# Performance work log

Hardware: AMD Instinct MI355X
Metric: run time of the kernel (lower is better)

The kernel has to match this reference:

```python
import jax, jax.numpy as jnp
import numpy as np

D_MODEL = 1024
NUM_HEADS = 16
D_K = D_MODEL // NUM_HEADS


def setup_inputs() -> dict:
    key = jax.random.key(0)
    ks = jax.random.split(key, 13)
    B, S = 2, 2048
    s = 1.0 / np.sqrt(D_MODEL)
    inp = {
        'q': jax.random.normal(ks[0], (B, S, D_MODEL), jnp.float32),
        'k': jax.random.normal(ks[1], (B, S, D_MODEL), jnp.float32),
        'v': jax.random.normal(ks[2], (B, S, D_MODEL), jnp.float32),
        'mask': jax.random.randint(ks[3], (B, S), 0, 2, jnp.int32),
        'Wq': jax.random.normal(ks[4], (D_MODEL, D_MODEL), jnp.float32) * s,
        'bq': jax.random.normal(ks[5], (D_MODEL,), jnp.float32) * s,
        'Wk': jax.random.normal(ks[6], (D_MODEL, D_MODEL), jnp.float32) * s,
        'bk': jax.random.normal(ks[7], (D_MODEL,), jnp.float32) * s,
        'Wv': jax.random.normal(ks[8], (D_MODEL, D_MODEL), jnp.float32) * s,
        'bv': jax.random.normal(ks[9], (D_MODEL,), jnp.float32) * s,
        'Wo': jax.random.normal(ks[10], (D_MODEL, D_MODEL), jnp.float32) * s,
        'bo': jax.random.normal(ks[11], (D_MODEL,), jnp.float32) * s,
    }
    return inp


def reference(q, k, v, mask, Wq, bq, Wk, bk, Wv, bv, Wo, bo):
    B, S, _ = q.shape

    def split(x):  # [B,S,D] -> [B,H,S,d_k]
        return x.reshape(B, -1, NUM_HEADS, D_K).transpose(0, 2, 1, 3)

    qh = split(q @ Wq.T + bq)
    kh = split(k @ Wk.T + bk)
    vh = split(v @ Wv.T + bv)

    scores = jnp.einsum('bhqd,bhkd->bhqk', qh, kh) / jnp.sqrt(jnp.float32(D_K))
    scores = jnp.where(mask[:, None, None, :] == 0, jnp.float32(-1e9), scores)
    attn = jax.nn.softmax(scores, axis=-1)
    out = jnp.einsum('bhqk,bhkd->bhqd', attn, vh)  # [B,H,S,d_k]
    out = out.transpose(0, 2, 1, 3).reshape(B, S, NUM_HEADS * D_K)
    return out @ Wo.T + bo
```

## Files before the change

### kernel.cpp

```cpp
#include <hip/hip_runtime.h>
#include <cstdint>
#include <cstddef>


using bf16   = __bf16;
using bf16x4 = __attribute__((ext_vector_type(4))) __bf16;
using bf16x8 = __attribute__((ext_vector_type(8))) __bf16;
using f32x4  = __attribute__((ext_vector_type(4))) float;

#define MFMA_BF16(a, b, c) __builtin_amdgcn_mfma_f32_16x16x32_bf16((a), (b), (c), 0, 0, 0)

__device__ __forceinline__ void gload_lds16(const void* g, void* l) {
  __builtin_amdgcn_global_load_lds((__attribute__((address_space(1))) void*)g,
                                   (__attribute__((address_space(3))) void*)l,
                                   16, 0, 0);
}

#define LOG2E 1.4426950408889634f

__global__ __launch_bounds__(256) void prep_kernel(
    const float* __restrict__ q, const float* __restrict__ k, const float* __restrict__ v,
    const int* __restrict__ mask,
    const float* __restrict__ Wq, const float* __restrict__ Wk,
    const float* __restrict__ Wv, const float* __restrict__ Wo,
    bf16* __restrict__ qb, bf16* __restrict__ kb, bf16* __restrict__ vb,
    bf16* __restrict__ Wqb, bf16* __restrict__ Wkb, bf16* __restrict__ Wvb,
    bf16* __restrict__ Wob, float* __restrict__ maskf)
{
  const int NQ = 1048576;
  const int NW = 262144;
  int i = blockIdx.x * 256 + threadIdx.x;
  if (i < 3 * NQ) {
    const float* src; bf16* dst; int j;
    if (i < NQ)        { src = q; dst = qb; j = i; }
    else if (i < 2*NQ) { src = k; dst = kb; j = i - NQ; }
    else               { src = v; dst = vb; j = i - 2*NQ; }
    float4 f = ((const float4*)src)[j];
    ((bf16x4*)dst)[j] = bf16x4{(bf16)f.x, (bf16)f.y, (bf16)f.z, (bf16)f.w};
  } else if (i < 3*NQ + 4*NW) {
    int j = i - 3*NQ;
    const float* src; bf16* dst;
    if (j < NW)        { src = Wq; dst = Wqb; }
    else if (j < 2*NW) { src = Wk; dst = Wkb; j -= NW; }
    else if (j < 3*NW) { src = Wv; dst = Wvb; j -= 2*NW; }
    else               { src = Wo; dst = Wob; j -= 3*NW; }
    float4 f = ((const float4*)src)[j];
    ((bf16x4*)dst)[j] = bf16x4{(bf16)f.x, (bf16)f.y, (bf16)f.z, (bf16)f.w};
  } else if (i < 3*NQ + 4*NW + 1024) {
    int j = i - 3*NQ - 4*NW;
    int4 mi = ((const int4*)mask)[j];
    float4 o;
    o.x = (mi.x == 0) ? -1e9f * LOG2E : 0.0f;
    o.y = (mi.y == 0) ? -1e9f * LOG2E : 0.0f;
    o.z = (mi.z == 0) ? -1e9f * LOG2E : 0.0f;
    o.w = (mi.w == 0) ? -1e9f * LOG2E : 0.0f;
    ((float4*)maskf)[j] = o;
  }
}

__global__ __launch_bounds__(256, 2) void proj3_kernel(
    const bf16* __restrict__ Xq, const bf16* __restrict__ Xk, const bf16* __restrict__ Xv,
    const bf16* __restrict__ Wqb, const bf16* __restrict__ Wkb, const bf16* __restrict__ Wvb,
    const float* __restrict__ bq, const float* __restrict__ bk, const float* __restrict__ bv,
    bf16* __restrict__ qh, bf16* __restrict__ kh, bf16* __restrict__ vhT)
{
  __shared__ bf16 As[256 * 64];
  __shared__ bf16 Bs[128 * 64];

  const int bid = blockIdx.x;
  const int z   = bid >> 7;
  const int r_  = bid & 127;

  const int tid = threadIdx.x, w = tid >> 6, lane = tid & 63;
  const int quad = lane >> 4, l16 = lane & 15;
  const int sw = l16 & 7;
  const int srow8 = lane >> 3;
  const int scol  = ((lane & 7) ^ srow8) * 8;

  const bf16* Aptr; const bf16* Bptr;
  int m0, n0;
  if (z == 2) { Aptr = Wvb; Bptr = Xv; m0 = (r_ >> 5) * 256; n0 = (r_ & 31) * 128; }
  else        { Aptr = (z == 0) ? Xq : Xk; Bptr = (z == 0) ? Wqb : Wkb;
                m0 = (r_ >> 3) * 256; n0 = (r_ & 7) * 128; }

  f32x4 acc[4][8];
#pragma unroll
  for (int mt = 0; mt < 4; ++mt)
#pragma unroll
    for (int nt = 0; nt < 8; ++nt)
      acc[mt][nt] = f32x4{0.f, 0.f, 0.f, 0.f};

  for (int k0 = 0; k0 < 1024; k0 += 64) {
#pragma unroll
    for (int c12 = 0; c12 < 12; ++c12) {
      const int c = w * 12 + c12;
      if (c < 32) {
        const int row = c * 8 + srow8;
        gload_lds16(Aptr + (size_t)(m0 + row) * 1024 + k0 + scol, As + c * 512);
      } else {
        const int cB = c - 32;
        const int row = cB * 8 + srow8;
        gload_lds16(Bptr + (size_t)(n0 + row) * 1024 + k0 + scol, Bs + cB * 512);
      }
    }
    __syncthreads();
#pragma unroll
    for (int kk = 0; kk < 2; ++kk) {
      bf16x8 af[4], bf[8];
#pragma unroll
      for (int mt = 0; mt < 4; ++mt)
        af[mt] = *(const bf16x8*)(As + (w*64 + mt*16 + l16) * 64 + ((kk*4 + quad) ^ sw) * 8);
#pragma unroll
      for (int nt = 0; nt < 8; ++nt)
        bf[nt] = *(const bf16x8*)(Bs + (nt*16 + l16) * 64 + ((kk*4 + quad) ^ sw) * 8);
#pragma unroll
      for (int mt = 0; mt < 4; ++mt)
#pragma unroll
        for (int nt = 0; nt < 8; ++nt)
          acc[mt][nt] = MFMA_BF16(af[mt], bf[nt], acc[mt][nt]);
    }
    __syncthreads();
  }

  if (z == 2) {
#pragma unroll
    for (int mt = 0; mt < 4; ++mt) {
      const int dvb = m0 + w*64 + mt*16 + quad*4;
      const float4 bv4 = *(const float4*)(bv + dvb);
#pragma unroll
      for (int nt = 0; nt < 8; ++nt) {
        const int tok = n0 + nt*16 + l16;
        const int bb = tok >> 11, s = tok & 2047;
#pragma unroll
        for (int r = 0; r < 4; ++r) {
          const int dv = dvb + r;
          const int h = dv >> 6, d = dv & 63;
          vhT[(((size_t)bb*16 + h)*64 + d)*2048 + s] = (bf16)(acc[mt][nt][r] + (&bv4.x)[r]);
        }
      }
    }
  } else {
    const float* bias = (z == 0) ? bq : bk;
#pragma unroll
    for (int mt = 0; mt < 4; ++mt) {
#pragma unroll
      for (int nt = 0; nt < 8; ++nt) {
        const int n = n0 + nt*16 + l16;
        const int h = n >> 6, d = n & 63;
        const float bn = bias[n];
#pragma unroll
        for (int r = 0; r < 4; ++r) {
          const int m  = m0 + w*64 + mt*16 + quad*4 + r;
          const int bb = m >> 11, s = m & 2047;
          const float val = acc[mt][nt][r] + bn;
          if (z == 0)
            qh[(((size_t)bb*16 + h)*2048 + s)*64 + d] = (bf16)(val * (0.125f * LOG2E));
          else
            kh[(((size_t)bb*16 + h)*2048 + s)*64 + d] = (bf16)val;
        }
      }
    }
  }
}

#define PSTRIDE 72

#define ATTN_BODY(T, FKC, FKN, MKC, MKN)                                        \
  {                                                                             \
    if ((T) < 30) stageTo((T) + 2, kvnn);                                       \
    if ((T) < 31) {                                                             \
      _Pragma("unroll")                                                         \
      for (int mb = 0; mb < 4; ++mb)                                            \
        MKN[mb] = *(const float4*)(mbase + ((T) + 1) * 64 + mb * 16);           \
      const char* pA = kvb + kvnxt + laneA;                                     \
      const char* pB = kvb + kvnxt + laneB;                                     \
      _Pragma("unroll")                                                         \
      for (int mb = 0; mb < 4; ++mb) {                                          \
        FKN[mb*2+0] = *(const bf16x8*)(pA + mb*2048);                           \
        FKN[mb*2+1] = *(const bf16x8*)(pB + mb*2048);                           \
      }                                                                         \
    }                                                                           \
    bf16x8 fV[8];                                                               \
    {                                                                           \
      const char* pA = kvb + kvcur + 8192 + laneA;                              \
      const char* pB = kvb + kvcur + 8192 + laneB;                              \
      _Pragma("unroll")                                                         \
      for (int mb = 0; mb < 4; ++mb) {                                          \
        fV[mb*2+0] = *(const bf16x8*)(pA + mb*2048);                            \
        fV[mb*2+1] = *(const bf16x8*)(pB + mb*2048);                            \
      }                                                                         \
    }                                                                           \
    _Pragma("unroll")                                                           \
    for (int rb = 0; rb < 2; ++rb) {                                            \
      f32x4 sac[4];                                                             \
      _Pragma("unroll")                                                         \
      for (int mb = 0; mb < 4; ++mb)                                            \
        sac[mb] = f32x4{MKC[mb].x, MKC[mb].y, MKC[mb].z, MKC[mb].w};            \
      _Pragma("unroll")                                                         \
      for (int kk = 0; kk < 2; ++kk)                                            \
        _Pragma("unroll")                                                       \
        for (int mb = 0; mb < 4; ++mb)                                          \
          sac[mb] = MFMA_BF16(FKC[mb*2+kk], aQ[rb][kk], sac[mb]);               \
      float p[4][4];                                                            \
      _Pragma("unroll")                                                         \
      for (int mb = 0; mb < 4; ++mb) {                                          \
        _Pragma("unroll")                                                       \
        for (int r = 0; r < 4; ++r) p[mb][r] = __builtin_amdgcn_exp2f(sac[mb][r]); \
        lacc[rb] += f32x4{p[mb][0], p[mb][1], p[mb][2], p[mb][3]};              \
      }                                                                         \
      bf16* bWr = rb ? bW1 : bW0;                                               \
      const bf16* bRr = rb ? bR1 : bR0;                                         \
      _Pragma("unroll")                                                         \
      for (int mb = 0; mb < 4; ++mb)                                            \
        *(bf16x4*)(bWr + mb*16) = bf16x4{(bf16)p[mb][0], (bf16)p[mb][1],        \
                                         (bf16)p[mb][2], (bf16)p[mb][3]};       \
      _Pragma("unroll")                                                         \
      for (int kk = 0; kk < 2; ++kk) {                                          \
        bf16x8 aP = *(const bf16x8*)(bRr + kk*32);                              \
        _Pragma("unroll")                                                       \
        for (int mb = 0; mb < 4; ++mb)                                          \
          Oacc[rb][mb] = MFMA_BF16(fV[mb*2+kk], aP, Oacc[rb][mb]);              \
      }                                                                         \
    }                                                                           \
    __syncthreads();                                                            \
    { int tmp_ = kvcur; kvcur = kvnxt; kvnxt = kvnn; kvnn = tmp_; }             \
  }

__global__ __launch_bounds__(256, 2) void attn_kernel(
    const bf16* __restrict__ qh, const bf16* __restrict__ kh,
    const bf16* __restrict__ vhT, const float* __restrict__ maskf,
    bf16* __restrict__ out)
{
  __shared__ bf16 KV[3][2][4096];
  __shared__ bf16 Ps[4][2][16 * PSTRIDE];

  const int tid = threadIdx.x, w = tid >> 6, lane = tid & 63;
  const int quad = lane >> 4, l16 = lane & 15;
  const int sw = l16 & 7;
  const int srow8 = lane >> 3;
  const int scol  = ((lane & 7) ^ srow8) * 8;

  const int L  = blockIdx.x;
  const int bh = (L & 7) + ((L >> 7) << 3);
  const int qt = (L >> 3) & 15;
  const int b  = bh >> 4, h = bh & 15;
  const int q0 = qt * 128 + w * 32;

  const bf16* kbase = kh  + (size_t)bh * 2048 * 64;
  const bf16* vbase = vhT + (size_t)bh * 64 * 2048;
  const bf16* qbase = qh  + ((size_t)bh * 2048 + q0) * 64;
  const float* mbase = maskf + (size_t)b * 2048 + quad * 4;

  char* kvb = (char*)&KV[0][0][0];

  auto stageTo = [&](int t, int bufoff) {
    const int kt0 = t * 64;
#pragma unroll
    for (int c2 = 0; c2 < 2; ++c2) {
      const int c   = w * 2 + c2;
      const int row = c * 8 + srow8;
      gload_lds16(kbase + (size_t)(kt0 + row) * 64 + scol, kvb + bufoff + c * 1024);
      gload_lds16(vbase + (size_t)row * 2048 + kt0 + scol, kvb + bufoff + 8192 + c * 1024);
    }
  };

  bf16x8 aQ[2][2];
#pragma unroll
  for (int rb = 0; rb < 2; ++rb)
#pragma unroll
    for (int kk = 0; kk < 2; ++kk)
      aQ[rb][kk] = *(const bf16x8*)(qbase + (size_t)(rb*16 + l16)*64 + kk*32 + quad*8);

  const int laneA = l16 * 128 + ((quad    ) ^ sw) * 16;
  const int laneB = l16 * 128 + ((quad + 4) ^ sw) * 16;
  bf16*       bW0 = &Ps[w][0][0] + l16 * PSTRIDE + quad * 4;
  const bf16* bR0 = &Ps[w][0][0] + l16 * PSTRIDE + quad * 8;
  bf16*       bW1 = &Ps[w][1][0] + l16 * PSTRIDE + quad * 4;
  const bf16* bR1 = &Ps[w][1][0] + l16 * PSTRIDE + quad * 8;

  f32x4 Oacc[2][4];
  f32x4 lacc[2];
#pragma unroll
  for (int rb = 0; rb < 2; ++rb) {
    lacc[rb] = f32x4{0.f, 0.f, 0.f, 0.f};
#pragma unroll
    for (int mb = 0; mb < 4; ++mb) Oacc[rb][mb] = f32x4{0.f, 0.f, 0.f, 0.f};
  }

  stageTo(0, 0);
  stageTo(1, 16384);
  float4 mkA[4], mkB[4];
#pragma unroll
  for (int mb = 0; mb < 4; ++mb) mkA[mb] = *(const float4*)(mbase + mb*16);
  __syncthreads();

  bf16x8 fKa[8], fKb[8];
  {
    const char* pA = kvb + laneA;
    const char* pB = kvb + laneB;
#pragma unroll
    for (int mb = 0; mb < 4; ++mb) {
      fKa[mb*2+0] = *(const bf16x8*)(pA + mb*2048);
      fKa[mb*2+1] = *(const bf16x8*)(pB + mb*2048);
    }
  }

  int kvcur = 0, kvnxt = 16384, kvnn = 32768;

  for (int tt = 0; tt < 32; tt += 2) {
    ATTN_BODY(tt,     fKa, fKb, mkA, mkB);
    ATTN_BODY(tt + 1, fKb, fKa, mkB, mkA);
  }

#pragma unroll
  for (int rb = 0; rb < 2; ++rb) {
    float l_ = lacc[rb][0] + lacc[rb][1] + lacc[rb][2] + lacc[rb][3];
    l_ += __shfl_xor(l_, 16);
    l_ += __shfl_xor(l_, 32);
    const float inv = 1.0f / l_;
#pragma unroll
    for (int mb = 0; mb < 4; ++mb) {
      bf16x4 o = bf16x4{(bf16)(Oacc[rb][mb][0]*inv), (bf16)(Oacc[rb][mb][1]*inv),
                        (bf16)(Oacc[rb][mb][2]*inv), (bf16)(Oacc[rb][mb][3]*inv)};
      *(bf16x4*)(out + ((size_t)b*2048 + q0 + rb*16 + l16)*1024 + h*64 + mb*16 + quad*4) = o;
    }
  }
}

__global__ __launch_bounds__(256) void oproj_kernel(
    const bf16* __restrict__ Ain, const bf16* __restrict__ Wob,
    const float* __restrict__ bo, float* __restrict__ out)
{
  __shared__ bf16 As[64 * 64];
  __shared__ bf16 Bs[128 * 64];
  const int m0 = blockIdx.x * 64, n0 = blockIdx.y * 128;

  const int tid = threadIdx.x, w = tid >> 6, lane = tid & 63;
  const int quad = lane >> 4, l16 = lane & 15;
  const int sw = l16 & 7;
  const int srow8 = lane >> 3;
  const int scol  = ((lane & 7) ^ srow8) * 8;

  f32x4 acc[4][2];
#pragma unroll
  for (int mt = 0; mt < 4; ++mt)
#pragma unroll
    for (int nt = 0; nt < 2; ++nt)
      acc[mt][nt] = f32x4{0.f, 0.f, 0.f, 0.f};

  for (int k0 = 0; k0 < 1024; k0 += 64) {
#pragma unroll
    for (int c4 = 0; c4 < 6; ++c4) {
      const int c = w * 6 + c4;
      if (c < 8) {
        const int row = c * 8 + srow8;
        gload_lds16(Ain + (size_t)(m0 + row) * 1024 + k0 + scol, As + c * 512);
      } else {
        const int cB = c - 8;
        const int row = cB * 8 + srow8;
        gload_lds16(Wob + (size_t)(n0 + row) * 1024 + k0 + scol, Bs + cB * 512);
      }
    }
    __syncthreads();
#pragma unroll
    for (int kk = 0; kk < 2; ++kk) {
      bf16x8 af[4], bfr[2];
#pragma unroll
      for (int mt = 0; mt < 4; ++mt)
        af[mt] = *(const bf16x8*)(As + (mt*16 + l16) * 64 + ((kk*4 + quad) ^ sw) * 8);
#pragma unroll
      for (int nt = 0; nt < 2; ++nt)
        bfr[nt] = *(const bf16x8*)(Bs + (w*32 + nt*16 + l16) * 64 + ((kk*4 + quad) ^ sw) * 8);
#pragma unroll
      for (int mt = 0; mt < 4; ++mt)
#pragma unroll
        for (int nt = 0; nt < 2; ++nt)
          acc[mt][nt] = MFMA_BF16(af[mt], bfr[nt], acc[mt][nt]);
    }
    __syncthreads();
  }

#pragma unroll
  for (int mt = 0; mt < 4; ++mt) {
#pragma unroll
    for (int nt = 0; nt < 2; ++nt) {
      const int n = n0 + w*32 + nt*16 + l16;
      const float bn = bo[n];
#pragma unroll
      for (int r = 0; r < 4; ++r) {
        const int m = m0 + mt*16 + quad*4 + r;
        out[(size_t)m * 1024 + n] = acc[mt][nt][r] + bn;
      }
    }
  }
}

extern "C" void kernel_launch(void* const* d_in, const int* in_sizes, int n_in,
                              void* d_out, int out_size, void* d_ws, size_t ws_size,
                              hipStream_t stream)
{
  const float* q    = (const float*)d_in[0];
  const float* k    = (const float*)d_in[1];
  const float* v    = (const float*)d_in[2];
  const int*   mask = (const int*)d_in[3];
  const float* Wq   = (const float*)d_in[4];
  const float* bq   = (const float*)d_in[5];
  const float* Wk   = (const float*)d_in[6];
  const float* bk   = (const float*)d_in[7];
  const float* Wv   = (const float*)d_in[8];
  const float* bv   = (const float*)d_in[9];
  const float* Wo   = (const float*)d_in[10];
  const float* bo   = (const float*)d_in[11];

  char* ws = (char*)d_ws;
  bf16*  qb    = (bf16*)(ws);
  bf16*  kb    = (bf16*)(ws + (8ull  << 20));
  bf16*  vb    = (bf16*)(ws + (16ull << 20));
  bf16*  Wqb   = (bf16*)(ws + (24ull << 20));
  bf16*  Wkb   = (bf16*)(ws + (26ull << 20));
  bf16*  Wvb   = (bf16*)(ws + (28ull << 20));
  bf16*  Wob   = (bf16*)(ws + (30ull << 20));
  float* maskf = (float*)(ws + (32ull << 20));
  bf16*  qh    = (bf16*)(ws + (33ull << 20));
  bf16*  kh    = (bf16*)(ws + (41ull << 20));
  bf16*  vhT   = (bf16*)(ws + (49ull << 20));
  bf16*  ao    = (bf16*)(ws);
  float* out   = (float*)d_out;

  prep_kernel<<<16388, 256, 0, stream>>>(q, k, v, mask, Wq, Wk, Wv, Wo,
                                         qb, kb, vb, Wqb, Wkb, Wvb, Wob, maskf);
  proj3_kernel<<<384, 256, 0, stream>>>(qb, kb, vb, Wqb, Wkb, Wvb,
                                        bq, bk, bv, qh, kh, vhT);
  attn_kernel<<<512, 256, 0, stream>>>(qh, kh, vhT, maskf, ao);
  oproj_kernel<<<dim3(64, 8), 256, 0, stream>>>(ao, Wob, bo, out);
}
```

Before: 222.7 us.

## Shrink projection tiles to 128x128 and keep attention P in registers

The QKV projection GEMM moves from 256x128 tiles with 1-D warps to 128x128 tiles with a 2x2 warp grid. This doubles the grid to 768 blocks and raises the occupancy hint to 3, trading less operand reuse per tile for better CU fill. In attention, the softmax probabilities are packed to bf16 with v_cvt_pk_bf16_f32 and rearranged into MFMA A-operand layout with permlane32/permlane16 swaps, instead of round-tripping through an LDS scratch buffer. This removes LDS writes, reads and the scratch allocation, at the cost of a few cross-lane ops. It relies on the permlane swap instructions being available on gfx950.

```diff
diff --git a/kernel.cpp b/kernel.cpp
--- a/kernel.cpp
+++ b/kernel.cpp
@@ -15,6 +15,13 @@
                                    (__attribute__((address_space(3))) void*)l,
                                    16, 0, 0);
 }
+
+#define CVT_PK(d, lo, hi) \
+  asm("v_cvt_pk_bf16_f32 %0, %1, %2" : "=v"(d) : "v"(lo), "v"(hi))
+#define SWAP32(x, y) \
+  asm("v_permlane32_swap_b32 %0, %1" : "+v"(x), "+v"(y))
+#define SWAP16(x, y) \
+  asm("v_permlane16_swap_b32 %0, %1" : "+v"(x), "+v"(y))
 
 #define LOG2E 1.4426950408889634f
 
@@ -58,20 +65,21 @@
   }
 }
 
-__global__ __launch_bounds__(256, 2) void proj3_kernel(
+__global__ __launch_bounds__(256, 3) void proj3_kernel(
     const bf16* __restrict__ Xq, const bf16* __restrict__ Xk, const bf16* __restrict__ Xv,
     const bf16* __restrict__ Wqb, const bf16* __restrict__ Wkb, const bf16* __restrict__ Wvb,
     const float* __restrict__ bq, const float* __restrict__ bk, const float* __restrict__ bv,
     bf16* __restrict__ qh, bf16* __restrict__ kh, bf16* __restrict__ vhT)
 {
-  __shared__ bf16 As[256 * 64];
+  __shared__ bf16 As[128 * 64];
   __shared__ bf16 Bs[128 * 64];
 
   const int bid = blockIdx.x;
-  const int z   = bid >> 7;
-  const int r_  = bid & 127;
+  const int z   = bid >> 8;
+  const int r_  = bid & 255;
 
   const int tid = threadIdx.x, w = tid >> 6, lane = tid & 63;
+  const int wr = w >> 1, wc = w & 1;
   const int quad = lane >> 4, l16 = lane & 15;
   const int sw = l16 & 7;
   const int srow8 = lane >> 3;
@@ -79,26 +87,26 @@
 
   const bf16* Aptr; const bf16* Bptr;
   int m0, n0;
-  if (z == 2) { Aptr = Wvb; Bptr = Xv; m0 = (r_ >> 5) * 256; n0 = (r_ & 31) * 128; }
+  if (z == 2) { Aptr = Wvb; Bptr = Xv; m0 = (r_ >> 5) * 128; n0 = (r_ & 31) * 128; }
   else        { Aptr = (z == 0) ? Xq : Xk; Bptr = (z == 0) ? Wqb : Wkb;
-                m0 = (r_ >> 3) * 256; n0 = (r_ & 7) * 128; }
-
-  f32x4 acc[4][8];
+                m0 = (r_ >> 3) * 128; n0 = (r_ & 7) * 128; }
+
+  f32x4 acc[4][4];
 #pragma unroll
   for (int mt = 0; mt < 4; ++mt)
 #pragma unroll
-    for (int nt = 0; nt < 8; ++nt)
+    for (int nt = 0; nt < 4; ++nt)
       acc[mt][nt] = f32x4{0.f, 0.f, 0.f, 0.f};
 
   for (int k0 = 0; k0 < 1024; k0 += 64) {
 #pragma unroll
-    for (int c12 = 0; c12 < 12; ++c12) {
-      const int c = w * 12 + c12;
-      if (c < 32) {
+    for (int c8 = 0; c8 < 8; ++c8) {
+      const int c = w * 8 + c8;
+      if (c < 16) {
         const int row = c * 8 + srow8;
         gload_lds16(Aptr + (size_t)(m0 + row) * 1024 + k0 + scol, As + c * 512);
       } else {
-        const int cB = c - 32;
+        const int cB = c - 16;
         const int row = cB * 8 + srow8;
         gload_lds16(Bptr + (size_t)(n0 + row) * 1024 + k0 + scol, Bs + cB * 512);
       }
@@ -106,17 +114,17 @@
     __syncthreads();
 #pragma unroll
     for (int kk = 0; kk < 2; ++kk) {
-      bf16x8 af[4], bf[8];
+      bf16x8 af[4], bf[4];
 #pragma unroll
       for (int mt = 0; mt < 4; ++mt)
-        af[mt] = *(const bf16x8*)(As + (w*64 + mt*16 + l16) * 64 + ((kk*4 + quad) ^ sw) * 8);
-#pragma unroll
-      for (int nt = 0; nt < 8; ++nt)
-        bf[nt] = *(const bf16x8*)(Bs + (nt*16 + l16) * 64 + ((kk*4 + quad) ^ sw) * 8);
+        af[mt] = *(const bf16x8*)(As + (wr*64 + mt*16 + l16) * 64 + ((kk*4 + quad) ^ sw) * 8);
+#pragma unroll
+      for (int nt = 0; nt < 4; ++nt)
+        bf[nt] = *(const bf16x8*)(Bs + (wc*64 + nt*16 + l16) * 64 + ((kk*4 + quad) ^ sw) * 8);
 #pragma unroll
       for (int mt = 0; mt < 4; ++mt)
 #pragma unroll
-        for (int nt = 0; nt < 8; ++nt)
+        for (int nt = 0; nt < 4; ++nt)
           acc[mt][nt] = MFMA_BF16(af[mt], bf[nt], acc[mt][nt]);
     }
     __syncthreads();
@@ -125,11 +133,11 @@
   if (z == 2) {
 #pragma unroll
     for (int mt = 0; mt < 4; ++mt) {
-      const int dvb = m0 + w*64 + mt*16 + quad*4;
+      const int dvb = m0 + wr*64 + mt*16 + quad*4;
       const float4 bv4 = *(const float4*)(bv + dvb);
 #pragma unroll
-      for (int nt = 0; nt < 8; ++nt) {
-        const int tok = n0 + nt*16 + l16;
+      for (int nt = 0; nt < 4; ++nt) {
+        const int tok = n0 + wc*64 + nt*16 + l16;
         const int bb = tok >> 11, s = tok & 2047;
 #pragma unroll
         for (int r = 0; r < 4; ++r) {
@@ -144,13 +152,13 @@
 #pragma unroll
     for (int mt = 0; mt < 4; ++mt) {
 #pragma unroll
-      for (int nt = 0; nt < 8; ++nt) {
-        const int n = n0 + nt*16 + l16;
+      for (int nt = 0; nt < 4; ++nt) {
+        const int n = n0 + wc*64 + nt*16 + l16;
         const int h = n >> 6, d = n & 63;
         const float bn = bias[n];
 #pragma unroll
         for (int r = 0; r < 4; ++r) {
-          const int m  = m0 + w*64 + mt*16 + quad*4 + r;
+          const int m  = m0 + wr*64 + mt*16 + quad*4 + r;
           const int bb = m >> 11, s = m & 2047;
           const float val = acc[mt][nt][r] + bn;
           if (z == 0)
@@ -163,7 +171,6 @@
   }
 }
 
-#define PSTRIDE 72
 
 #define ATTN_BODY(T, FKC, FKN, MKC, MKN)                                        \
   {                                                                             \
@@ -208,18 +215,23 @@
         for (int r = 0; r < 4; ++r) p[mb][r] = __builtin_amdgcn_exp2f(sac[mb][r]); \
         lacc[rb] += f32x4{p[mb][0], p[mb][1], p[mb][2], p[mb][3]};              \
       }                                                                         \
-      bf16* bWr = rb ? bW1 : bW0;                                               \
-      const bf16* bRr = rb ? bR1 : bR0;                                         \
-      _Pragma("unroll")                                                         \
-      for (int mb = 0; mb < 4; ++mb)                                            \
-        *(bf16x4*)(bWr + mb*16) = bf16x4{(bf16)p[mb][0], (bf16)p[mb][1],        \
-                                         (bf16)p[mb][2], (bf16)p[mb][3]};       \
+      uint32_t pk0[4], pk1[4];                                                  \
+      _Pragma("unroll")                                                         \
+      for (int mb = 0; mb < 4; ++mb) {                                          \
+        CVT_PK(pk0[mb], p[mb][0], p[mb][1]);                                    \
+        CVT_PK(pk1[mb], p[mb][2], p[mb][3]);                                    \
+      }                                                                         \
       _Pragma("unroll")                                                         \
       for (int kk = 0; kk < 2; ++kk) {                                          \
-        bf16x8 aP = *(const bf16x8*)(bRr + kk*32);                              \
+        uint32_t a0 = pk0[2*kk], b0 = pk0[2*kk+1];                              \
+        uint32_t a1 = pk1[2*kk], b1 = pk1[2*kk+1];                              \
+        SWAP32(a0, b0); SWAP16(a0, b0);                                         \
+        SWAP32(a1, b1); SWAP16(a1, b1);                                         \
+        union { uint32_t u[4]; bf16x8 v; } un;                                  \
+        un.u[0] = a0; un.u[1] = a1; un.u[2] = b0; un.u[3] = b1;                 \
         _Pragma("unroll")                                                       \
         for (int mb = 0; mb < 4; ++mb)                                          \
-          Oacc[rb][mb] = MFMA_BF16(fV[mb*2+kk], aP, Oacc[rb][mb]);              \
+          Oacc[rb][mb] = MFMA_BF16(fV[mb*2+kk], un.v, Oacc[rb][mb]);            \
       }                                                                         \
     }                                                                           \
     __syncthreads();                                                            \
@@ -232,7 +244,6 @@
     bf16* __restrict__ out)
 {
   __shared__ bf16 KV[3][2][4096];
-  __shared__ bf16 Ps[4][2][16 * PSTRIDE];
 
   const int tid = threadIdx.x, w = tid >> 6, lane = tid & 63;
   const int quad = lane >> 4, l16 = lane & 15;
@@ -273,10 +284,6 @@
 
   const int laneA = l16 * 128 + ((quad    ) ^ sw) * 16;
   const int laneB = l16 * 128 + ((quad + 4) ^ sw) * 16;
-  bf16*       bW0 = &Ps[w][0][0] + l16 * PSTRIDE + quad * 4;
-  const bf16* bR0 = &Ps[w][0][0] + l16 * PSTRIDE + quad * 8;
-  bf16*       bW1 = &Ps[w][1][0] + l16 * PSTRIDE + quad * 4;
-  const bf16* bR1 = &Ps[w][1][0] + l16 * PSTRIDE + quad * 8;
 
   f32x4 Oacc[2][4];
   f32x4 lacc[2];
@@ -429,7 +436,7 @@
 
   prep_kernel<<<16388, 256, 0, stream>>>(q, k, v, mask, Wq, Wk, Wv, Wo,
                                          qb, kb, vb, Wqb, Wkb, Wvb, Wob, maskf);
-  proj3_kernel<<<384, 256, 0, stream>>>(qb, kb, vb, Wqb, Wkb, Wvb,
+  proj3_kernel<<<768, 256, 0, stream>>>(qb, kb, vb, Wqb, Wkb, Wvb,
                                         bq, bk, bv, qh, kh, vhT);
   attn_kernel<<<512, 256, 0, stream>>>(qh, kh, vhT, maskf, ao);
   oproj_kernel<<<dim3(64, 8), 256, 0, stream>>>(ao, Wob, bo, out);
```

New measurement: 215.7 us. 1.03x faster.
